# Kernel tuning notes

Measured on AMD Instinct MI355X. Metric: run time of the kernel, lower is better.

The kernel has to match this reference:

```python
import jax, jax.numpy as jnp
import numpy as np

N_NODES = 50000
N_EDGES = 800000
F_IN = 128
HIDDEN = 128
N_CLASSES = 40


def setup_inputs() -> dict:
    key = jax.random.key(0)
    k1, k2, k3, k4 = jax.random.split(key, 4)
    features = jax.random.normal(k1, (N_NODES, F_IN), dtype=jnp.float32)
    edge_index = jax.random.randint(k2, (2, N_EDGES), 0, N_NODES, dtype=jnp.int64)
    # Glorot-style init for the GCNConv linear weights, zero bias (PyG default)
    W1 = jax.random.normal(k3, (F_IN, HIDDEN), dtype=jnp.float32) * (1.0 / np.sqrt(F_IN))
    b1 = jnp.zeros((HIDDEN,), dtype=jnp.float32)
    W2 = jax.random.normal(k4, (HIDDEN, N_CLASSES), dtype=jnp.float32) * (1.0 / np.sqrt(HIDDEN))
    b2 = jnp.zeros((N_CLASSES,), dtype=jnp.float32)
    return {"features": features, "edge_index": edge_index,
            "W1": W1, "b1": b1, "W2": W2, "b2": b2}


def _gcn_norm(edge_index, num_nodes):
    # Add self-loops and compute symmetric normalization D^-1/2 (A+I) D^-1/2
    loop = jnp.arange(num_nodes, dtype=edge_index.dtype)
    src = jnp.concatenate([edge_index[0], loop])  # [E+N]
    dst = jnp.concatenate([edge_index[1], loop])  # [E+N]
    w = jnp.ones(src.shape[0], dtype=jnp.float32)
    deg = jax.ops.segment_sum(w, dst, num_segments=num_nodes)  # [N]
    dinv = jnp.where(deg > 0, jax.lax.rsqrt(deg), 0.0)
    norm = dinv[src] * w * dinv[dst]  # [E+N]
    return src, dst, norm


def _gcn_conv(x, W, b, src, dst, norm, num_nodes):
    h = x @ W  # linear transform first (PyG GCNConv): [N, out]
    msg = h[src] * norm[:, None]  # gather + scale: [E+N, out]
    out = jax.ops.segment_sum(msg, dst, num_segments=num_nodes)  # scatter-add
    return out + b


def reference(features, edge_index, W1, b1, W2, b2):
    n = features.shape[0]
    src, dst, norm = _gcn_norm(edge_index, n)
    x = jax.nn.relu(_gcn_conv(features, W1, b1, src, dst, norm, n))
    # dropout is identity at eval time (training=False)
    x = _gcn_conv(x, W2, b2, src, dst, norm, n)
    return jax.nn.log_softmax(x, axis=1)
```

## Files before the change

### kernel.cpp

```cpp
#include <hip/hip_runtime.h>
#include <hip/hip_bf16.h>
#include <math.h>

#define N_NODES 50000
#define N_EDGES 800000

#define SCAN_CHUNK 512
#define SCAN_NB ((N_NODES + SCAN_CHUNK - 1) / SCAN_CHUNK)

__global__ __launch_bounds__(256) void count_kernel(const int* __restrict__ ei,
                                                    int* __restrict__ cnt) {
  int e = blockIdx.x * 256 + threadIdx.x;
  if (e < N_EDGES) {
    int d = ei[N_EDGES + e];
    d = min(max(d, 0), N_NODES - 1);
    atomicAdd(&cnt[d], 1);
  }
}

__global__ __launch_bounds__(256) void scan_reduce(const int* __restrict__ cnt,
                                                   int* __restrict__ bsum) {
  __shared__ int s[256];
  int t = threadIdx.x;
  int i0 = blockIdx.x * SCAN_CHUNK + t * 2;
  int v = 0;
  if (i0 < N_NODES) v += cnt[i0];
  if (i0 + 1 < N_NODES) v += cnt[i0 + 1];
  s[t] = v;
  __syncthreads();
  for (int off = 128; off > 0; off >>= 1) {
    if (t < off) s[t] += s[t + off];
    __syncthreads();
  }
  if (t == 0) bsum[blockIdx.x] = s[0];
}

__global__ void scan_block(int* bsum) {
  __shared__ int s[128];
  int t = threadIdx.x;
  int v = (t < SCAN_NB) ? bsum[t] : 0;
  s[t] = v;
  __syncthreads();
  for (int off = 1; off < 128; off <<= 1) {
    int a = (t >= off) ? s[t - off] : 0;
    __syncthreads();
    s[t] += a;
    __syncthreads();
  }
  if (t < SCAN_NB) bsum[t] = s[t] - v;
}

__global__ __launch_bounds__(256) void scan_final(const int* __restrict__ cnt,
                                                  const int* __restrict__ bsum,
                                                  int* __restrict__ rowptr,
                                                  int* __restrict__ cursor,
                                                  float* __restrict__ dinv) {
  __shared__ int s[256];
  int t = threadIdx.x;
  int b = blockIdx.x;
  int i0 = b * SCAN_CHUNK + t * 2;
  int c0 = (i0 < N_NODES) ? cnt[i0] : 0;
  int c1 = (i0 + 1 < N_NODES) ? cnt[i0 + 1] : 0;
  int v = c0 + c1;
  s[t] = v;
  __syncthreads();
  for (int off = 1; off < 256; off <<= 1) {
    int a = (t >= off) ? s[t - off] : 0;
    __syncthreads();
    s[t] += a;
    __syncthreads();
  }
  int excl = s[t] - v + bsum[b];
  if (i0 < N_NODES) {
    rowptr[i0] = excl;
    cursor[i0] = excl;
    dinv[i0] = rsqrtf((float)(c0 + 1));
  }
  if (i0 + 1 < N_NODES) {
    rowptr[i0 + 1] = excl + c0;
    cursor[i0 + 1] = excl + c0;
    dinv[i0 + 1] = rsqrtf((float)(c1 + 1));
  }
  if (b == 0 && t == 0) rowptr[N_NODES] = N_EDGES;
}

__global__ __launch_bounds__(256) void fill_kernel(const int* __restrict__ ei,
                                                   int* __restrict__ cursor,
                                                   int* __restrict__ col) {
  int e = blockIdx.x * 256 + threadIdx.x;
  if (e >= N_EDGES) return;
  int srcv = ei[e];
  int dstv = ei[N_EDGES + e];
  srcv = min(max(srcv, 0), N_NODES - 1);
  dstv = min(max(dstv, 0), N_NODES - 1);
  int p = atomicAdd(&cursor[dstv], 1);
  col[p] = srcv;
}

__global__ __launch_bounds__(256) void gemm1_kernel(const float* __restrict__ X,
                                                    const float* __restrict__ W,
                                                    const float* __restrict__ dinv,
                                                    __hip_bfloat16* __restrict__ h1p) {
  __shared__ float xs[128 * 64];
  __shared__ float ws[128 * 64];
  int t = threadIdx.x;
  int row0 = blockIdx.x * 128;
  int wv = t >> 6, lane = t & 63;
  int wr = (wv >> 1) << 6, wc = (wv & 1) << 6;
  int tr = lane >> 3, tc = lane & 7;
  float acc[8][8];
#pragma unroll
  for (int i = 0; i < 8; ++i)
#pragma unroll
    for (int m = 0; m < 8; ++m) acc[i][m] = 0.f;

  for (int h = 0; h < 2; ++h) {
    if (h) __syncthreads();
#pragma unroll
    for (int it = 0; it < 8; ++it) {
      int idx = t + it * 256;
      int r = idx >> 4, kq = idx & 15;
      int gr = row0 + r;
      if (gr >= N_NODES) gr = N_NODES - 1;
      float4 v = *(const float4*)(X + (size_t)gr * 128 + h * 64 + kq * 4);
      *(float4*)(xs + r * 64 + ((kq ^ (r & 7)) << 2)) = v;
    }
#pragma unroll
    for (int it = 0; it < 8; ++it) {
      int idx = t + it * 256;
      int k = idx >> 5, jq = idx & 31;
      float4 v = *(const float4*)(W + (size_t)(h * 64 + k) * 128 + jq * 4);
      int kc = k >> 2, kr = k & 3;
      int j0 = jq * 4;
      ws[(j0 + 0) * 64 + (((kc ^ ((j0 + 0) & 7)) << 2) | kr)] = v.x;
      ws[(j0 + 1) * 64 + (((kc ^ ((j0 + 1) & 7)) << 2) | kr)] = v.y;
      ws[(j0 + 2) * 64 + (((kc ^ ((j0 + 2) & 7)) << 2) | kr)] = v.z;
      ws[(j0 + 3) * 64 + (((kc ^ ((j0 + 3) & 7)) << 2) | kr)] = v.w;
    }
    __syncthreads();
    for (int kq = 0; kq < 16; ++kq) {
      float4 xv[8], wvv[8];
#pragma unroll
      for (int i = 0; i < 8; ++i)
        xv[i] = *(const float4*)(xs + (wr + tr + 8 * i) * 64 + ((kq ^ tr) << 2));
#pragma unroll
      for (int m = 0; m < 8; ++m)
        wvv[m] = *(const float4*)(ws + (wc + tc + 8 * m) * 64 + ((kq ^ tc) << 2));
#pragma unroll
      for (int i = 0; i < 8; ++i)
#pragma unroll
        for (int m = 0; m < 8; ++m) {
          acc[i][m] = fmaf(xv[i].x, wvv[m].x, acc[i][m]);
          acc[i][m] = fmaf(xv[i].y, wvv[m].y, acc[i][m]);
          acc[i][m] = fmaf(xv[i].z, wvv[m].z, acc[i][m]);
          acc[i][m] = fmaf(xv[i].w, wvv[m].w, acc[i][m]);
        }
    }
  }
#pragma unroll
  for (int i = 0; i < 8; ++i) {
    int gr = row0 + wr + tr + 8 * i;
    if (gr < N_NODES) {
      float di = dinv[gr];
#pragma unroll
      for (int m = 0; m < 8; ++m)
        h1p[(size_t)gr * 128 + wc + tc + 8 * m] = __float2bfloat16(di * acc[i][m]);
    }
  }
}

__global__ __launch_bounds__(256) void agg1_kernel(const __hip_bfloat16* __restrict__ h1p,
                                                   const int* __restrict__ rowptr,
                                                   const int* __restrict__ col,
                                                   const float* __restrict__ dinv,
                                                   const float* __restrict__ b1,
                                                   float* __restrict__ x2) {
  int wid = (blockIdx.x * 256 + threadIdx.x) >> 6;
  int lane = threadIdx.x & 63;
  if (wid >= N_NODES) return;
  int rs = rowptr[wid], re = rowptr[wid + 1];
  int q = lane >> 4;
  int fl = lane & 15;
  const uint4* hp = (const uint4*)h1p;
  float a0[8], a1[8];
#pragma unroll
  for (int j = 0; j < 8; ++j) { a0[j] = 0.f; a1[j] = 0.f; }

#define ACC_BF16(A, U)                                                        \
  {                                                                           \
    uint4 u_ = (U);                                                           \
    A[0] += __uint_as_float(u_.x << 16);                                      \
    A[1] += __uint_as_float(u_.x & 0xffff0000u);                              \
    A[2] += __uint_as_float(u_.y << 16);                                      \
    A[3] += __uint_as_float(u_.y & 0xffff0000u);                              \
    A[4] += __uint_as_float(u_.z << 16);                                      \
    A[5] += __uint_as_float(u_.z & 0xffff0000u);                              \
    A[6] += __uint_as_float(u_.w << 16);                                      \
    A[7] += __uint_as_float(u_.w & 0xffff0000u);                              \
  }

  if (q == 0) ACC_BF16(a0, hp[(size_t)wid * 16 + fl]);

  for (int base = rs; base < re; base += 64) {
    int idx = base + lane;
    int c = (idx < re) ? col[idx] : 0;
    int nb = min(64, re - base);
    int e = 0;
    for (; e + 8 <= nb; e += 8) {
      int s0 = __shfl(c, e + q);
      int s1 = __shfl(c, e + 4 + q);
      uint4 u0 = hp[(size_t)s0 * 16 + fl];
      uint4 u1 = hp[(size_t)s1 * 16 + fl];
      ACC_BF16(a0, u0);
      ACC_BF16(a1, u1);
    }
    for (; e < nb; e += 4) {
      if (e + q < nb) {
        int s0 = __shfl(c, e + q);
        ACC_BF16(a0, hp[(size_t)s0 * 16 + fl]);
      }
    }
  }
#undef ACC_BF16

#pragma unroll
  for (int j = 0; j < 8; ++j) {
    float v = a0[j] + a1[j];
    v += __shfl_xor(v, 16);
    v += __shfl_xor(v, 32);
    a0[j] = v;
  }
  if (q == 0) {
    float di = dinv[wid];
    float4 bb0 = ((const float4*)b1)[fl * 2];
    float4 bb1 = ((const float4*)b1)[fl * 2 + 1];
    float4 o0, o1;
    o0.x = fmaxf(fmaf(di, a0[0], bb0.x), 0.f);
    o0.y = fmaxf(fmaf(di, a0[1], bb0.y), 0.f);
    o0.z = fmaxf(fmaf(di, a0[2], bb0.z), 0.f);
    o0.w = fmaxf(fmaf(di, a0[3], bb0.w), 0.f);
    o1.x = fmaxf(fmaf(di, a0[4], bb1.x), 0.f);
    o1.y = fmaxf(fmaf(di, a0[5], bb1.y), 0.f);
    o1.z = fmaxf(fmaf(di, a0[6], bb1.z), 0.f);
    o1.w = fmaxf(fmaf(di, a0[7], bb1.w), 0.f);
    *(float4*)(x2 + (size_t)wid * 128 + fl * 8) = o0;
    *(float4*)(x2 + (size_t)wid * 128 + fl * 8 + 4) = o1;
  }
}

__global__ __launch_bounds__(256) void gemm2_kernel(const float* __restrict__ X2,
                                                    const float* __restrict__ W2,
                                                    const float* __restrict__ dinv,
                                                    float* __restrict__ h2p) {
  __shared__ float xs[64 * 128];
  __shared__ float ws[40 * 128];
  int t = threadIdx.x;
  int row0 = blockIdx.x * 64;
#pragma unroll
  for (int it = 0; it < 8; ++it) {
    int idx = t + it * 256;
    int r = idx >> 5, kq = idx & 31;
    int gr = row0 + r;
    if (gr >= N_NODES) gr = N_NODES - 1;
    float4 v = *(const float4*)(X2 + (size_t)gr * 128 + kq * 4);
    *(float4*)(xs + r * 128 + ((kq ^ (r & 7)) << 2)) = v;
  }
  for (int idx = t; idx < 1280; idx += 256) {
    int k = idx / 10, jq = idx % 10;
    float4 v = *(const float4*)(W2 + k * 40 + jq * 4);
    int kc = k >> 2, kr = k & 3;
    int j0 = jq * 4;
    ws[(j0 + 0) * 128 + (((kc ^ ((j0 + 0) & 7)) << 2) | kr)] = v.x;
    ws[(j0 + 1) * 128 + (((kc ^ ((j0 + 1) & 7)) << 2) | kr)] = v.y;
    ws[(j0 + 2) * 128 + (((kc ^ ((j0 + 2) & 7)) << 2) | kr)] = v.z;
    ws[(j0 + 3) * 128 + (((kc ^ ((j0 + 3) & 7)) << 2) | kr)] = v.w;
  }
  __syncthreads();
  int wv = t >> 6, lane = t & 63;
  int tr = lane >> 3, tc = lane & 7;
  int rbase = wv * 16;
  float acc[2][5];
#pragma unroll
  for (int i = 0; i < 2; ++i)
#pragma unroll
    for (int m = 0; m < 5; ++m) acc[i][m] = 0.f;
  for (int kq = 0; kq < 32; ++kq) {
    float4 xv[2], wvv[5];
#pragma unroll
    for (int i = 0; i < 2; ++i)
      xv[i] = *(const float4*)(xs + (rbase + tr + 8 * i) * 128 + ((kq ^ tr) << 2));
#pragma unroll
    for (int m = 0; m < 5; ++m)
      wvv[m] = *(const float4*)(ws + (tc + 8 * m) * 128 + ((kq ^ tc) << 2));
#pragma unroll
    for (int i = 0; i < 2; ++i)
#pragma unroll
      for (int m = 0; m < 5; ++m) {
        acc[i][m] = fmaf(xv[i].x, wvv[m].x, acc[i][m]);
        acc[i][m] = fmaf(xv[i].y, wvv[m].y, acc[i][m]);
        acc[i][m] = fmaf(xv[i].z, wvv[m].z, acc[i][m]);
        acc[i][m] = fmaf(xv[i].w, wvv[m].w, acc[i][m]);
      }
  }
#pragma unroll
  for (int i = 0; i < 2; ++i) {
    int gr = row0 + rbase + tr + 8 * i;
    if (gr < N_NODES) {
      float di = dinv[gr];
#pragma unroll
      for (int m = 0; m < 5; ++m)
        h2p[(size_t)gr * 48 + tc + 8 * m] = di * acc[i][m];
    }
  }
}

__global__ __launch_bounds__(256) void agg2_softmax_kernel(const float* __restrict__ h2p,
                                                           const int* __restrict__ rowptr,
                                                           const int* __restrict__ col,
                                                           const float* __restrict__ dinv,
                                                           const float* __restrict__ b2,
                                                           float* __restrict__ out) {
  int wid = (blockIdx.x * 256 + threadIdx.x) >> 6;
  int lane = threadIdx.x & 63;
  if (wid >= N_NODES) return;
  int rs = rowptr[wid], re = rowptr[wid + 1];
  bool act = lane < 40;
  float ac0 = act ? h2p[(size_t)wid * 48 + lane] : 0.f;
  float ac1 = 0.f, ac2 = 0.f, ac3 = 0.f;
  for (int base = rs; base < re; base += 64) {
    int idx = base + lane;
    int c = (idx < re) ? col[idx] : 0;
    int nb = min(64, re - base);
    int e = 0;
    for (; e + 4 <= nb; e += 4) {
      int s0 = __shfl(c, e), s1 = __shfl(c, e + 1);
      int s2 = __shfl(c, e + 2), s3 = __shfl(c, e + 3);
      if (act) {
        ac0 += h2p[(size_t)s0 * 48 + lane];
        ac1 += h2p[(size_t)s1 * 48 + lane];
        ac2 += h2p[(size_t)s2 * 48 + lane];
        ac3 += h2p[(size_t)s3 * 48 + lane];
      }
    }
    for (; e < nb; ++e) {
      int s0 = __shfl(c, e);
      if (act) ac0 += h2p[(size_t)s0 * 48 + lane];
    }
  }
  float acc = (ac0 + ac1) + (ac2 + ac3);
  float v = act ? fmaf(dinv[wid], acc, b2[lane]) : -1e30f;
  float m = v;
#pragma unroll
  for (int off = 32; off > 0; off >>= 1) m = fmaxf(m, __shfl_xor(m, off));
  float ex = act ? expf(v - m) : 0.f;
  float ssum = ex;
#pragma unroll
  for (int off = 32; off > 0; off >>= 1) ssum += __shfl_xor(ssum, off);
  float ls = logf(ssum);
  if (act) out[(size_t)wid * 40 + lane] = v - m - ls;
}

extern "C" void kernel_launch(void* const* d_in, const int* in_sizes, int n_in,
                              void* d_out, int out_size, void* d_ws, size_t ws_size,
                              hipStream_t stream) {
  const float* X = (const float*)d_in[0];
  const int* ei = (const int*)d_in[1];
  const float* W1 = (const float*)d_in[2];
  const float* b1 = (const float*)d_in[3];
  const float* W2 = (const float*)d_in[4];
  const float* b2 = (const float*)d_in[5];
  float* out = (float*)d_out;

  char* p = (char*)d_ws;
  auto carve = [&](size_t bytes) -> void* {
    void* q = (void*)p;
    p += (bytes + 255) & ~(size_t)255;
    return q;
  };
  __hip_bfloat16* h1p = (__hip_bfloat16*)carve((size_t)N_NODES * 128 * 2);
  float* x2 = (float*)carve((size_t)N_NODES * 128 * 4);
  float* h2p = (float*)carve((size_t)N_NODES * 48 * 4);
  int* col = (int*)carve((size_t)N_EDGES * 4);
  int* cnt = (int*)carve((size_t)N_NODES * 4);
  int* rowptr = (int*)carve((size_t)(N_NODES + 1) * 4);
  int* cursor = (int*)carve((size_t)N_NODES * 4);
  float* dinv = (float*)carve((size_t)N_NODES * 4);
  int* bsum = (int*)carve((size_t)SCAN_NB * 4);

  hipMemsetAsync(cnt, 0, (size_t)N_NODES * 4, stream);
  count_kernel<<<(N_EDGES + 255) / 256, 256, 0, stream>>>(ei, cnt);
  scan_reduce<<<SCAN_NB, 256, 0, stream>>>(cnt, bsum);
  scan_block<<<1, 128, 0, stream>>>(bsum);
  scan_final<<<SCAN_NB, 256, 0, stream>>>(cnt, bsum, rowptr, cursor, dinv);
  fill_kernel<<<(N_EDGES + 255) / 256, 256, 0, stream>>>(ei, cursor, col);
  gemm1_kernel<<<(N_NODES + 127) / 128, 256, 0, stream>>>(X, W1, dinv, h1p);
  agg1_kernel<<<(N_NODES + 3) / 4, 256, 0, stream>>>(h1p, rowptr, col, dinv, b1, x2);
  gemm2_kernel<<<(N_NODES + 63) / 64, 256, 0, stream>>>(x2, W2, dinv, h2p);
  agg2_softmax_kernel<<<(N_NODES + 3) / 4, 256, 0, stream>>>(h2p, rowptr, col, dinv, b2, out);
}
```

Measured before the change: 296.2 us.

## Merge gemm1 with degree counting and move source dinv scaling into aggregation

The first-layer GEMM no longer needs dinv, so it now runs in the same launch as the edge-count kernel, with extra blocks doing the atomic counting. This removes one launch and lets the GEMM overlap the degree computation. In exchange, agg1 loads dinv[col] for every edge and applies it per neighbor with FMAs instead of plain adds. The stored bf16 features are now unscaled, which changes rounding slightly.

```diff
diff --git a/kernel.cpp b/kernel.cpp
--- a/kernel.cpp
+++ b/kernel.cpp
@@ -8,13 +8,87 @@
 #define SCAN_CHUNK 512
 #define SCAN_NB ((N_NODES + SCAN_CHUNK - 1) / SCAN_CHUNK)
 
-__global__ __launch_bounds__(256) void count_kernel(const int* __restrict__ ei,
-                                                    int* __restrict__ cnt) {
-  int e = blockIdx.x * 256 + threadIdx.x;
-  if (e < N_EDGES) {
-    int d = ei[N_EDGES + e];
-    d = min(max(d, 0), N_NODES - 1);
-    atomicAdd(&cnt[d], 1);
+#define GEMM1_NB ((N_NODES + 127) / 128)
+#define COUNT_NB ((N_EDGES + 255) / 256)
+
+__global__ __launch_bounds__(256) void gemm1_count_kernel(
+    const float* __restrict__ X, const float* __restrict__ W,
+    __hip_bfloat16* __restrict__ h1u,
+    const int* __restrict__ ei, int* __restrict__ cnt) {
+  __shared__ float xs[128 * 64];
+  __shared__ float ws[128 * 64];
+  int bid = blockIdx.x;
+  int t = threadIdx.x;
+  if (bid >= GEMM1_NB) {
+    int e = (bid - GEMM1_NB) * 256 + t;
+    if (e < N_EDGES) {
+      int d = ei[N_EDGES + e];
+      d = min(max(d, 0), N_NODES - 1);
+      atomicAdd(&cnt[d], 1);
+    }
+    return;
+  }
+  int row0 = bid * 128;
+  int wv = t >> 6, lane = t & 63;
+  int wr = (wv >> 1) << 6, wc = (wv & 1) << 6;
+  int tr = lane >> 3, tc = lane & 7;
+  float acc[8][8];
+#pragma unroll
+  for (int i = 0; i < 8; ++i)
+#pragma unroll
+    for (int m = 0; m < 8; ++m) acc[i][m] = 0.f;
+
+  for (int h = 0; h < 2; ++h) {
+    if (h) __syncthreads();
+#pragma unroll
+    for (int it = 0; it < 8; ++it) {
+      int idx = t + it * 256;
+      int r = idx >> 4, kq = idx & 15;
+      int gr = row0 + r;
+      if (gr >= N_NODES) gr = N_NODES - 1;
+      float4 v = *(const float4*)(X + (size_t)gr * 128 + h * 64 + kq * 4);
+      *(float4*)(xs + r * 64 + ((kq ^ (r & 7)) << 2)) = v;
+    }
+#pragma unroll
+    for (int it = 0; it < 8; ++it) {
+      int idx = t + it * 256;
+      int k = idx >> 5, jq = idx & 31;
+      float4 v = *(const float4*)(W + (size_t)(h * 64 + k) * 128 + jq * 4);
+      int kc = k >> 2, kr = k & 3;
+      int j0 = jq * 4;
+      ws[(j0 + 0) * 64 + (((kc ^ ((j0 + 0) & 7)) << 2) | kr)] = v.x;
+      ws[(j0 + 1) * 64 + (((kc ^ ((j0 + 1) & 7)) << 2) | kr)] = v.y;
+      ws[(j0 + 2) * 64 + (((kc ^ ((j0 + 2) & 7)) << 2) | kr)] = v.z;
+      ws[(j0 + 3) * 64 + (((kc ^ ((j0 + 3) & 7)) << 2) | kr)] = v.w;
+    }
+    __syncthreads();
+    for (int kq = 0; kq < 16; ++kq) {
+      float4 xv[8], wvv[8];
+#pragma unroll
+      for (int i = 0; i < 8; ++i)
+        xv[i] = *(const float4*)(xs + (wr + tr + 8 * i) * 64 + ((kq ^ tr) << 2));
+#pragma unroll
+      for (int m = 0; m < 8; ++m)
+        wvv[m] = *(const float4*)(ws + (wc + tc + 8 * m) * 64 + ((kq ^ tc) << 2));
+#pragma unroll
+      for (int i = 0; i < 8; ++i)
+#pragma unroll
+        for (int m = 0; m < 8; ++m) {
+          acc[i][m] = fmaf(xv[i].x, wvv[m].x, acc[i][m]);
+          acc[i][m] = fmaf(xv[i].y, wvv[m].y, acc[i][m]);
+          acc[i][m] = fmaf(xv[i].z, wvv[m].z, acc[i][m]);
+          acc[i][m] = fmaf(xv[i].w, wvv[m].w, acc[i][m]);
+        }
+    }
+  }
+#pragma unroll
+  for (int i = 0; i < 8; ++i) {
+    int gr = row0 + wr + tr + 8 * i;
+    if (gr < N_NODES) {
+#pragma unroll
+      for (int m = 0; m < 8; ++m)
+        h1u[(size_t)gr * 128 + wc + tc + 8 * m] = __float2bfloat16(acc[i][m]);
+    }
   }
 }
 
@@ -97,79 +171,7 @@
   col[p] = srcv;
 }
 
-__global__ __launch_bounds__(256) void gemm1_kernel(const float* __restrict__ X,
-                                                    const float* __restrict__ W,
-                                                    const float* __restrict__ dinv,
-                                                    __hip_bfloat16* __restrict__ h1p) {
-  __shared__ float xs[128 * 64];
-  __shared__ float ws[128 * 64];
-  int t = threadIdx.x;
-  int row0 = blockIdx.x * 128;
-  int wv = t >> 6, lane = t & 63;
-  int wr = (wv >> 1) << 6, wc = (wv & 1) << 6;
-  int tr = lane >> 3, tc = lane & 7;
-  float acc[8][8];
-#pragma unroll
-  for (int i = 0; i < 8; ++i)
-#pragma unroll
-    for (int m = 0; m < 8; ++m) acc[i][m] = 0.f;
-
-  for (int h = 0; h < 2; ++h) {
-    if (h) __syncthreads();
-#pragma unroll
-    for (int it = 0; it < 8; ++it) {
-      int idx = t + it * 256;
-      int r = idx >> 4, kq = idx & 15;
-      int gr = row0 + r;
-      if (gr >= N_NODES) gr = N_NODES - 1;
-      float4 v = *(const float4*)(X + (size_t)gr * 128 + h * 64 + kq * 4);
-      *(float4*)(xs + r * 64 + ((kq ^ (r & 7)) << 2)) = v;
-    }
-#pragma unroll
-    for (int it = 0; it < 8; ++it) {
-      int idx = t + it * 256;
-      int k = idx >> 5, jq = idx & 31;
-      float4 v = *(const float4*)(W + (size_t)(h * 64 + k) * 128 + jq * 4);
-      int kc = k >> 2, kr = k & 3;
-      int j0 = jq * 4;
-      ws[(j0 + 0) * 64 + (((kc ^ ((j0 + 0) & 7)) << 2) | kr)] = v.x;
-      ws[(j0 + 1) * 64 + (((kc ^ ((j0 + 1) & 7)) << 2) | kr)] = v.y;
-      ws[(j0 + 2) * 64 + (((kc ^ ((j0 + 2) & 7)) << 2) | kr)] = v.z;
-      ws[(j0 + 3) * 64 + (((kc ^ ((j0 + 3) & 7)) << 2) | kr)] = v.w;
-    }
-    __syncthreads();
-    for (int kq = 0; kq < 16; ++kq) {
-      float4 xv[8], wvv[8];
-#pragma unroll
-      for (int i = 0; i < 8; ++i)
-        xv[i] = *(const float4*)(xs + (wr + tr + 8 * i) * 64 + ((kq ^ tr) << 2));
-#pragma unroll
-      for (int m = 0; m < 8; ++m)
-        wvv[m] = *(const float4*)(ws + (wc + tc + 8 * m) * 64 + ((kq ^ tc) << 2));
-#pragma unroll
-      for (int i = 0; i < 8; ++i)
-#pragma unroll
-        for (int m = 0; m < 8; ++m) {
-          acc[i][m] = fmaf(xv[i].x, wvv[m].x, acc[i][m]);
-          acc[i][m] = fmaf(xv[i].y, wvv[m].y, acc[i][m]);
-          acc[i][m] = fmaf(xv[i].z, wvv[m].z, acc[i][m]);
-          acc[i][m] = fmaf(xv[i].w, wvv[m].w, acc[i][m]);
-        }
-    }
-  }
-#pragma unroll
-  for (int i = 0; i < 8; ++i) {
-    int gr = row0 + wr + tr + 8 * i;
-    if (gr < N_NODES) {
-      float di = dinv[gr];
-#pragma unroll
-      for (int m = 0; m < 8; ++m)
-        h1p[(size_t)gr * 128 + wc + tc + 8 * m] = __float2bfloat16(di * acc[i][m]);
-    }
-  }
-}
-
-__global__ __launch_bounds__(256) void agg1_kernel(const __hip_bfloat16* __restrict__ h1p,
+__global__ __launch_bounds__(256) void agg1_kernel(const __hip_bfloat16* __restrict__ h1u,
                                                    const int* __restrict__ rowptr,
                                                    const int* __restrict__ col,
                                                    const float* __restrict__ dinv,
@@ -181,47 +183,53 @@
   int rs = rowptr[wid], re = rowptr[wid + 1];
   int q = lane >> 4;
   int fl = lane & 15;
-  const uint4* hp = (const uint4*)h1p;
+  const uint4* hp = (const uint4*)h1u;
+  float diw = dinv[wid];
   float a0[8], a1[8];
 #pragma unroll
   for (int j = 0; j < 8; ++j) { a0[j] = 0.f; a1[j] = 0.f; }
 
-#define ACC_BF16(A, U)                                                        \
+#define ACC_BF16_W(A, U, Wt)                                                  \
   {                                                                           \
     uint4 u_ = (U);                                                           \
-    A[0] += __uint_as_float(u_.x << 16);                                      \
-    A[1] += __uint_as_float(u_.x & 0xffff0000u);                              \
-    A[2] += __uint_as_float(u_.y << 16);                                      \
-    A[3] += __uint_as_float(u_.y & 0xffff0000u);                              \
-    A[4] += __uint_as_float(u_.z << 16);                                      \
-    A[5] += __uint_as_float(u_.z & 0xffff0000u);                              \
-    A[6] += __uint_as_float(u_.w << 16);                                      \
-    A[7] += __uint_as_float(u_.w & 0xffff0000u);                              \
-  }
-
-  if (q == 0) ACC_BF16(a0, hp[(size_t)wid * 16 + fl]);
+    float w_ = (Wt);                                                          \
+    A[0] = fmaf(w_, __uint_as_float(u_.x << 16), A[0]);                       \
+    A[1] = fmaf(w_, __uint_as_float(u_.x & 0xffff0000u), A[1]);               \
+    A[2] = fmaf(w_, __uint_as_float(u_.y << 16), A[2]);                       \
+    A[3] = fmaf(w_, __uint_as_float(u_.y & 0xffff0000u), A[3]);               \
+    A[4] = fmaf(w_, __uint_as_float(u_.z << 16), A[4]);                       \
+    A[5] = fmaf(w_, __uint_as_float(u_.z & 0xffff0000u), A[5]);               \
+    A[6] = fmaf(w_, __uint_as_float(u_.w << 16), A[6]);                       \
+    A[7] = fmaf(w_, __uint_as_float(u_.w & 0xffff0000u), A[7]);               \
+  }
+
+  if (q == 0) ACC_BF16_W(a0, hp[(size_t)wid * 16 + fl], diw);
 
   for (int base = rs; base < re; base += 64) {
     int idx = base + lane;
     int c = (idx < re) ? col[idx] : 0;
+    float dv = (idx < re) ? dinv[c] : 0.f;
     int nb = min(64, re - base);
     int e = 0;
     for (; e + 8 <= nb; e += 8) {
       int s0 = __shfl(c, e + q);
       int s1 = __shfl(c, e + 4 + q);
+      float d0 = __shfl(dv, e + q);
+      float d1 = __shfl(dv, e + 4 + q);
       uint4 u0 = hp[(size_t)s0 * 16 + fl];
       uint4 u1 = hp[(size_t)s1 * 16 + fl];
-      ACC_BF16(a0, u0);
-      ACC_BF16(a1, u1);
+      ACC_BF16_W(a0, u0, d0);
+      ACC_BF16_W(a1, u1, d1);
     }
     for (; e < nb; e += 4) {
       if (e + q < nb) {
         int s0 = __shfl(c, e + q);
-        ACC_BF16(a0, hp[(size_t)s0 * 16 + fl]);
+        float d0 = __shfl(dv, e + q);
+        ACC_BF16_W(a0, hp[(size_t)s0 * 16 + fl], d0);
       }
     }
   }
-#undef ACC_BF16
+#undef ACC_BF16_W
 
 #pragma unroll
   for (int j = 0; j < 8; ++j) {
@@ -231,18 +239,17 @@
     a0[j] = v;
   }
   if (q == 0) {
-    float di = dinv[wid];
     float4 bb0 = ((const float4*)b1)[fl * 2];
     float4 bb1 = ((const float4*)b1)[fl * 2 + 1];
     float4 o0, o1;
-    o0.x = fmaxf(fmaf(di, a0[0], bb0.x), 0.f);
-    o0.y = fmaxf(fmaf(di, a0[1], bb0.y), 0.f);
-    o0.z = fmaxf(fmaf(di, a0[2], bb0.z), 0.f);
-    o0.w = fmaxf(fmaf(di, a0[3], bb0.w), 0.f);
-    o1.x = fmaxf(fmaf(di, a0[4], bb1.x), 0.f);
-    o1.y = fmaxf(fmaf(di, a0[5], bb1.y), 0.f);
-    o1.z = fmaxf(fmaf(di, a0[6], bb1.z), 0.f);
-    o1.w = fmaxf(fmaf(di, a0[7], bb1.w), 0.f);
+    o0.x = fmaxf(fmaf(diw, a0[0], bb0.x), 0.f);
+    o0.y = fmaxf(fmaf(diw, a0[1], bb0.y), 0.f);
+    o0.z = fmaxf(fmaf(diw, a0[2], bb0.z), 0.f);
+    o0.w = fmaxf(fmaf(diw, a0[3], bb0.w), 0.f);
+    o1.x = fmaxf(fmaf(diw, a0[4], bb1.x), 0.f);
+    o1.y = fmaxf(fmaf(diw, a0[5], bb1.y), 0.f);
+    o1.z = fmaxf(fmaf(diw, a0[6], bb1.z), 0.f);
+    o1.w = fmaxf(fmaf(diw, a0[7], bb1.w), 0.f);
     *(float4*)(x2 + (size_t)wid * 128 + fl * 8) = o0;
     *(float4*)(x2 + (size_t)wid * 128 + fl * 8 + 4) = o1;
   }
@@ -377,7 +384,7 @@
     p += (bytes + 255) & ~(size_t)255;
     return q;
   };
-  __hip_bfloat16* h1p = (__hip_bfloat16*)carve((size_t)N_NODES * 128 * 2);
+  __hip_bfloat16* h1u = (__hip_bfloat16*)carve((size_t)N_NODES * 128 * 2);
   float* x2 = (float*)carve((size_t)N_NODES * 128 * 4);
   float* h2p = (float*)carve((size_t)N_NODES * 48 * 4);
   int* col = (int*)carve((size_t)N_EDGES * 4);
@@ -388,13 +395,12 @@
   int* bsum = (int*)carve((size_t)SCAN_NB * 4);
 
   hipMemsetAsync(cnt, 0, (size_t)N_NODES * 4, stream);
-  count_kernel<<<(N_EDGES + 255) / 256, 256, 0, stream>>>(ei, cnt);
+  gemm1_count_kernel<<<GEMM1_NB + COUNT_NB, 256, 0, stream>>>(X, W1, h1u, ei, cnt);
   scan_reduce<<<SCAN_NB, 256, 0, stream>>>(cnt, bsum);
   scan_block<<<1, 128, 0, stream>>>(bsum);
   scan_final<<<SCAN_NB, 256, 0, stream>>>(cnt, bsum, rowptr, cursor, dinv);
   fill_kernel<<<(N_EDGES + 255) / 256, 256, 0, stream>>>(ei, cursor, col);
-  gemm1_kernel<<<(N_NODES + 127) / 128, 256, 0, stream>>>(X, W1, dinv, h1p);
-  agg1_kernel<<<(N_NODES + 3) / 4, 256, 0, stream>>>(h1p, rowptr, col, dinv, b1, x2);
+  agg1_kernel<<<(N_NODES + 3) / 4, 256, 0, stream>>>(h1u, rowptr, col, dinv, b1, x2);
   gemm2_kernel<<<(N_NODES + 63) / 64, 256, 0, stream>>>(x2, W2, dinv, h2p);
   agg2_softmax_kernel<<<(N_NODES + 3) / 4, 256, 0, stream>>>(h2p, rowptr, col, dinv, b2, out);
 }
```

After: 268.8 us. 1.1x faster.
